# Performance work log

Measured on AMD Instinct MI355X. Metric: run time of the kernel, lower is better.

Reference implementation:

```python
import jax, jax.numpy as jnp
import numpy as np

E, C, H, W = 64, 8, 32, 32  # E zonotope rows (1 center + 63 error terms)


def setup_inputs() -> dict:
    key = jax.random.key(0)
    x = jax.random.normal(key, (E, C, H, W), dtype=jnp.float32)
    # Zero center => lower < 0 < upper everywhere, so every element crosses
    # and the number of new error terms equals C*H*W (fixed output shape).
    x = x.at[0].set(0.0)
    return {"x": x}


def reference(x):
    e = x.shape[0]
    content_shape = x.shape[1:]
    n = int(np.prod(content_shape))  # max possible new error terms

    err = jnp.sum(jnp.abs(x[1:]), axis=0)
    upper = x[0] + err
    lower = x[0] - err

    cross = (lower * upper < 0).astype(x.dtype)   # crossing-zero mask
    nonneg = (lower >= 0).astype(x.dtype)         # strictly positive mask

    lam = nonneg + cross * upper / (upper - lower)
    lam = jnp.where(jnp.isnan(lam), 0.5, lam)
    # torch assigns lambda via .data (detached from the autograd graph)
    lam = jax.lax.stop_gradient(lam)

    delta = jnp.maximum(-lam * lower, (1.0 - lam) * upper)

    head = (delta / 2 + lam * x[0]) * cross + x[0] * nonneg          # new center
    body = x[1:] * (lam * cross + nonneg)                            # scaled old error terms

    # Vectorized stream-compaction scatter replacing the scripted .item() loop:
    # element k (flat order) with cross==True goes to tail row cumsum(cross)[k]-1.
    flat_cond = cross.reshape(-1) > 0
    vals = (delta / 2).reshape(-1)
    rows = jnp.cumsum(flat_cond.astype(jnp.int32)) - 1
    rows = jnp.clip(rows, 0, n - 1)
    tail = jnp.zeros((n, n), dtype=x.dtype)
    # (row, col) pairs are unique per column; masked-out elements write 0 (no-op).
    tail = tail.at[rows, jnp.arange(n)].set(jnp.where(flat_cond, vals, 0.0))

    return jnp.concatenate(
        [head[None], body, tail.reshape((n,) + content_shape)], axis=0
    )
```

## Files before the change

kernel.cpp:

```cpp
#include <hip/hip_runtime.h>
#include <math.h>

#define EROWS 64
#define NCOL  8192
#define TAIL_OFF (EROWS * NCOL)
#define TAIL_F4 (NCOL * NCOL / 4)
#define ROW_F4  (NCOL / 4)

#define WS_VAL(ws)     ((float*)(ws))
#define WS_FLAG(ws)    ((int*)((char*)(ws) + 32768))
#define WS_COLOF(ws)   ((int*)((char*)(ws) + 65536))
#define WS_TAILVAL(ws) ((float*)((char*)(ws) + 98304))
#define WS_COUNT(ws)   ((int*)((char*)(ws) + 131072))

__global__ __launch_bounds__(64) void headbody_kernel(const float* __restrict__ x,
                                float* __restrict__ out,
                                float* __restrict__ val,
                                int* __restrict__ flag) {
    int k = blockIdx.x * 64 + threadIdx.x;

    float err = 0.f;
#pragma unroll
    for (int e = 1; e < EROWS; ++e)
        err += fabsf(x[e * NCOL + k]);

    float x0    = x[k];
    float upper = x0 + err;
    float lower = x0 - err;

    float cross  = (lower * upper < 0.f) ? 1.f : 0.f;
    float nonneg = (lower >= 0.f) ? 1.f : 0.f;

    float lam = nonneg + cross * upper / (upper - lower);
    if (isnan(lam)) lam = 0.5f;

    float delta = fmaxf(-lam * lower, (1.f - lam) * upper);

    out[k] = (delta * 0.5f + lam * x0) * cross + x0 * nonneg;

    float scale = lam * cross + nonneg;
    val[k]  = delta * 0.5f;
    flag[k] = (cross > 0.f) ? 1 : 0;

#pragma unroll
    for (int e = 1; e < EROWS; ++e)
        out[e * NCOL + k] = x[e * NCOL + k] * scale;
}

__global__ __launch_bounds__(1024) void scan_kernel(const float* __restrict__ val,
                            const int* __restrict__ flag,
                            int* __restrict__ colof,
                            float* __restrict__ tailval,
                            int* __restrict__ count) {
    const int t    = threadIdx.x;
    const int lane = t & 63;
    const int wid  = t >> 6;

    int4 a = ((const int4*)flag)[t * 2 + 0];
    int4 b = ((const int4*)flag)[t * 2 + 1];
    int f[8] = {a.x, a.y, a.z, a.w, b.x, b.y, b.z, b.w};

    int s = 0;
#pragma unroll
    for (int j = 0; j < 8; ++j) s += f[j];

    int isc = s;
#pragma unroll
    for (int off = 1; off < 64; off <<= 1) {
        int v = __shfl_up(isc, off);
        if (lane >= off) isc += v;
    }

    __shared__ int wsum[16];
    if (lane == 63) wsum[wid] = isc;
    __syncthreads();

    int base = 0;
    for (int w = 0; w < wid; ++w) base += wsum[w];

    int running = base + isc - s;
    const int kbase = t * 8;
#pragma unroll
    for (int j = 0; j < 8; ++j) {
        if (f[j]) {
            colof[running]   = kbase + j;
            tailval[running] = val[kbase + j];
            ++running;
        }
    }
    if (t == 1023) *count = base + isc;
}

__global__ __launch_bounds__(256) void tail_kernel(const int* __restrict__ colof,
                           const float* __restrict__ tailval,
                           const int* __restrict__ count,
                           float* __restrict__ out) {
    const int t    = threadIdx.x;
    const int row0 = blockIdx.x * 4;
    const int cnt  = *count;
    float4* tail = (float4*)out + TAIL_OFF / 4;

#pragma unroll
    for (int j = 0; j < 4; ++j) {
        int   r   = row0 + j;
        int   col = (r < cnt) ? colof[r]   : -1;
        float tv  = (r < cnt) ? tailval[r] : 0.f;
        float4* rowp = tail + (size_t)r * ROW_F4;
#pragma unroll
        for (int i = 0; i < 8; ++i) {
            int c0 = (t + i * 256) << 2;
            float4 v;
            v.x = (col == c0 + 0) ? tv : 0.f;
            v.y = (col == c0 + 1) ? tv : 0.f;
            v.z = (col == c0 + 2) ? tv : 0.f;
            v.w = (col == c0 + 3) ? tv : 0.f;
            rowp[t + i * 256] = v;
        }
    }
}

extern "C" void kernel_launch(void* const* d_in, const int* in_sizes, int n_in,
                              void* d_out, int out_size, void* d_ws, size_t ws_size,
                              hipStream_t stream) {
    const float* x = (const float*)d_in[0];
    float* out = (float*)d_out;

    headbody_kernel<<<NCOL / 64, 64, 0, stream>>>(x, out, WS_VAL(d_ws), WS_FLAG(d_ws));
    scan_kernel<<<1, 1024, 0, stream>>>(WS_VAL(d_ws), WS_FLAG(d_ws),
                                        WS_COLOF(d_ws), WS_TAILVAL(d_ws), WS_COUNT(d_ws));
    tail_kernel<<<NCOL / 4, 256, 0, stream>>>(WS_COLOF(d_ws), WS_TAILVAL(d_ws),
                                              WS_COUNT(d_ws), out);
}
```

Measured before the change: 271.6 us.

## Zero-fill tail alongside head/body kernel and scatter diagonal values from scan

Fold the tail zero-fill into the head/body launch, with 2048 extra blocks writing zeros across the 256 MB tail. The scan kernel now writes each crossing value straight to its (row, column) slot, so the separate tail kernel and its colof/tailval/count workspace go away. This removes one launch and the per-element compare/select in the tail write while keeping the same total store traffic. The fill and head/body blocks share one grid, so their memory traffic can overlap. The scan still runs afterward on a single block, so its scattered writes stay correctly ordered after the zero-fill.

```diff
diff --git a/kernel.cpp b/kernel.cpp
--- a/kernel.cpp
+++ b/kernel.cpp
@@ -5,19 +5,30 @@
 #define NCOL  8192
 #define TAIL_OFF (EROWS * NCOL)
 #define TAIL_F4 (NCOL * NCOL / 4)
-#define ROW_F4  (NCOL / 4)
+#define FILL_BLOCKS 2048
+#define HB_BLOCKS   32
 
 #define WS_VAL(ws)     ((float*)(ws))
 #define WS_FLAG(ws)    ((int*)((char*)(ws) + 32768))
-#define WS_COLOF(ws)   ((int*)((char*)(ws) + 65536))
-#define WS_TAILVAL(ws) ((float*)((char*)(ws) + 98304))
-#define WS_COUNT(ws)   ((int*)((char*)(ws) + 131072))
 
-__global__ __launch_bounds__(64) void headbody_kernel(const float* __restrict__ x,
-                                float* __restrict__ out,
-                                float* __restrict__ val,
-                                int* __restrict__ flag) {
-    int k = blockIdx.x * 64 + threadIdx.x;
+
+__global__ __launch_bounds__(256) void fused_kernel(const float* __restrict__ x,
+                              float* __restrict__ out,
+                              float* __restrict__ val,
+                              int* __restrict__ flag) {
+    const int t = threadIdx.x;
+
+    if (blockIdx.x < FILL_BLOCKS) {
+        float4* tail = (float4*)out + TAIL_OFF / 4;
+        size_t base = (size_t)blockIdx.x * 8192;
+        float4 z;  z.x = 0.f; z.y = 0.f; z.z = 0.f; z.w = 0.f;
+#pragma unroll
+        for (int i = 0; i < 32; ++i)
+            tail[base + i * 256 + t] = z;
+        return;
+    }
+
+    int k = (blockIdx.x - FILL_BLOCKS) * 256 + t;
 
     float err = 0.f;
 #pragma unroll
@@ -49,9 +60,7 @@
 
 __global__ __launch_bounds__(1024) void scan_kernel(const float* __restrict__ val,
                             const int* __restrict__ flag,
-                            int* __restrict__ colof,
-                            float* __restrict__ tailval,
-                            int* __restrict__ count) {
+                            float* __restrict__ out) {
     const int t    = threadIdx.x;
     const int lane = t & 63;
     const int wid  = t >> 6;
@@ -80,41 +89,16 @@
 
     int running = base + isc - s;
     const int kbase = t * 8;
+    float* tail = out + TAIL_OFF;
 #pragma unroll
     for (int j = 0; j < 8; ++j) {
+        int k = kbase + j;
         if (f[j]) {
-            colof[running]   = kbase + j;
-            tailval[running] = val[kbase + j];
+            int r = running;
+            r = (r < 0) ? 0 : r;
+            r = (r > NCOL - 1) ? (NCOL - 1) : r;
+            tail[(size_t)r * NCOL + k] = val[k];
             ++running;
-        }
-    }
-    if (t == 1023) *count = base + isc;
-}
-
-__global__ __launch_bounds__(256) void tail_kernel(const int* __restrict__ colof,
-                           const float* __restrict__ tailval,
-                           const int* __restrict__ count,
-                           float* __restrict__ out) {
-    const int t    = threadIdx.x;
-    const int row0 = blockIdx.x * 4;
-    const int cnt  = *count;
-    float4* tail = (float4*)out + TAIL_OFF / 4;
-
-#pragma unroll
-    for (int j = 0; j < 4; ++j) {
-        int   r   = row0 + j;
-        int   col = (r < cnt) ? colof[r]   : -1;
-        float tv  = (r < cnt) ? tailval[r] : 0.f;
-        float4* rowp = tail + (size_t)r * ROW_F4;
-#pragma unroll
-        for (int i = 0; i < 8; ++i) {
-            int c0 = (t + i * 256) << 2;
-            float4 v;
-            v.x = (col == c0 + 0) ? tv : 0.f;
-            v.y = (col == c0 + 1) ? tv : 0.f;
-            v.z = (col == c0 + 2) ? tv : 0.f;
-            v.w = (col == c0 + 3) ? tv : 0.f;
-            rowp[t + i * 256] = v;
         }
     }
 }
@@ -125,9 +109,6 @@
     const float* x = (const float*)d_in[0];
     float* out = (float*)d_out;
 
-    headbody_kernel<<<NCOL / 64, 64, 0, stream>>>(x, out, WS_VAL(d_ws), WS_FLAG(d_ws));
-    scan_kernel<<<1, 1024, 0, stream>>>(WS_VAL(d_ws), WS_FLAG(d_ws),
-                                        WS_COLOF(d_ws), WS_TAILVAL(d_ws), WS_COUNT(d_ws));
-    tail_kernel<<<NCOL / 4, 256, 0, stream>>>(WS_COLOF(d_ws), WS_TAILVAL(d_ws),
-                                              WS_COUNT(d_ws), out);
+    fused_kernel<<<FILL_BLOCKS + HB_BLOCKS, 256, 0, stream>>>(x, out, WS_VAL(d_ws), WS_FLAG(d_ws));
+    scan_kernel<<<1, 1024, 0, stream>>>(WS_VAL(d_ws), WS_FLAG(d_ws), out);
 }
```

Measured after the change: 271.5 us. No clear change (-0.0%).
